# Kernel optimization log

Hardware: AMD Instinct MI355X
Metric: run time of the kernel (lower is better)

The kernel has to match this reference:

```python
import jax, jax.numpy as jnp
import numpy as np

DIM = 1024
N_SRC = 4096
N_TGT = 4096


def setup_inputs() -> dict:
    key = jax.random.key(0)
    ks = jax.random.split(key, 7)
    scale = 1.0 / np.sqrt(DIM)
    return {
        "source": jax.random.normal(ks[0], (N_SRC, DIM), dtype=jnp.float32),
        "target": jax.random.normal(ks[1], (N_TGT, DIM), dtype=jnp.float32),
        "W_src": jax.random.uniform(ks[2], (DIM, DIM), minval=-scale, maxval=scale, dtype=jnp.float32),
        "b_src": jax.random.uniform(ks[3], (DIM,), minval=-scale, maxval=scale, dtype=jnp.float32),
        "W_tgt": jax.random.uniform(ks[4], (DIM, DIM), minval=-scale, maxval=scale, dtype=jnp.float32),
        "b_tgt": jax.random.uniform(ks[5], (DIM,), minval=-scale, maxval=scale, dtype=jnp.float32),
        "temperature": jnp.array(1.0, dtype=jnp.float32),
    }


def reference(source, target, W_src, b_src, W_tgt, b_tgt, temperature):
    # Linear projections (torch Linear: x @ W.T + b)
    sp = source @ W_src.T + b_src            # [N, d]
    tp = target @ W_tgt.T + b_tgt            # [M, d]
    sq_s = jnp.sum(sp * sp, axis=-1, keepdims=True)   # [N, 1]
    sq_t = jnp.sum(tp * tp, axis=-1)                  # [M]
    d2 = sq_s + sq_t[None, :] - 2.0 * (sp @ tp.T)     # [N, M]
    cost = jnp.sqrt(jnp.maximum(d2, 0.0))
    # Softmin-style kernel, row-normalized over target entries
    K = jnp.exp(-cost / temperature)
    K = K / jnp.sum(K, axis=1, keepdims=True)
    aligned_source = K @ target                       # [N, d]
    return aligned_source, K
```

## Files before the change

### kernel.cpp

```cpp
#include <hip/hip_runtime.h>
#include <stdint.h>

#define DIM  1024
#define NSRC 4096
#define NTGT 4096

typedef __bf16 bf16_t;
typedef bf16_t bf16x8 __attribute__((ext_vector_type(8)));
typedef float  fx4    __attribute__((ext_vector_type(4)));

static __device__ __forceinline__ unsigned short f2bf(float f) {
  union { float f; uint32_t u; } v; v.f = f;
  return (unsigned short)((v.u + 0x7FFFu + ((v.u >> 16) & 1u)) >> 16);
}
static __device__ __forceinline__ float bf2f(unsigned short h) {
  union { uint32_t u; float f; } v; v.u = ((uint32_t)h) << 16;
  return v.f;
}

static __device__ __forceinline__ void gl_lds16(const unsigned short* g, unsigned short* l) {
  __builtin_amdgcn_global_load_lds(
      (__attribute__((address_space(1))) const void*)g,
      (__attribute__((address_space(3))) void*)l, 16, 0, 0);
}

typedef const __attribute__((address_space(3))) unsigned short* lds3p;

template <int IMM>
static __device__ __forceinline__ bf16x8 dsr128(lds3p p) {
  bf16x8 r;
  asm volatile("ds_read_b128 %0, %1 offset:%2" : "=v"(r) : "v"(p), "n"(IMM));
  return r;
}


__global__ void k_convert_all(const float* __restrict__ s, const float* __restrict__ t,
                              const float* __restrict__ w0, const float* __restrict__ w1,
                              unsigned short* __restrict__ sb, unsigned short* __restrict__ tb,
                              unsigned short* __restrict__ wb0, unsigned short* __restrict__ wb1) {
  int b = blockIdx.x;
  const float* in; unsigned short* out; int idx;
  if (b < 4096)      { in = s;  out = sb;  idx = b * 256 + threadIdx.x; }
  else if (b < 8192) { in = t;  out = tb;  idx = (b - 4096) * 256 + threadIdx.x; }
  else if (b < 9216) { in = w0; out = wb0; idx = (b - 8192) * 256 + threadIdx.x; }
  else               { in = w1; out = wb1; idx = (b - 9216) * 256 + threadIdx.x; }
  float4 v = ((const float4*)in)[idx];
  ushort4 o;
  o.x = f2bf(v.x); o.y = f2bf(v.y); o.z = f2bf(v.z); o.w = f2bf(v.w);
  ((ushort4*)out)[idx] = o;
}

__global__ void k_transpose_bf16(const float* __restrict__ in, unsigned short* __restrict__ out,
                                 int R, int C) {
  __shared__ unsigned short tile[32][33];
  int c0 = blockIdx.x * 32, r0 = blockIdx.y * 32;
  int tx = threadIdx.x, ty = threadIdx.y;
  for (int i = ty; i < 32; i += 8) {
    int row = r0 + i;
    int p = row & 63;
    int tr = (row & ~63) | ((p >> 2) | ((p & 3) << 4));
    tile[i][tx] = f2bf(in[(size_t)tr * C + c0 + tx]);
  }
  __syncthreads();
  for (int i = ty; i < 32; i += 8)
    out[(size_t)(c0 + i) * R + r0 + tx] = tile[tx][i];
}

__global__ void k_finalize_aligned(const float* __restrict__ P, float* __restrict__ aligned,
                                   const float* __restrict__ rs) {
  const int b = blockIdx.x;
  const int lane = threadIdx.x & 63, w = threadIdx.x >> 6;
  const int src = ((lane & 15) << 2) | (lane >> 4);
  const size_t stride = (size_t)NSRC * DIM;
#pragma unroll
  for (int it = 0; it < 4; ++it) {
    int idx = b * 16 + w * 4 + it;
    size_t base = (size_t)idx * 64;
    float r = 1.0f / rs[idx >> 4];
    float v = (P[base + lane] + P[base + stride + lane] +
               P[base + 2 * stride + lane] + P[base + 3 * stride + lane]) * r;
    aligned[base + lane] = __shfl(v, src, 64);
  }
}

__global__ void k_finalize_K(const unsigned short* __restrict__ Eb, float* __restrict__ Kf,
                             const float* __restrict__ rs) {
  const int b = blockIdx.x;
  const int lane = threadIdx.x & 63, w = threadIdx.x >> 6;
  const int src = ((lane & 15) << 2) | (lane >> 4);
#pragma unroll
  for (int it = 0; it < 8; ++it) {
    int idx = b * 32 + w * 8 + it;
    size_t base = (size_t)idx * 64;
    float r = 1.0f / rs[idx >> 6];
    float v = bf2f(Eb[base + lane]) * r;
    Kf[base + lane] = __shfl(v, src, 64);
  }
}

template <int EPI, int LDK>
__global__ void __launch_bounds__(512, 2)
k_tile256(const unsigned short* __restrict__ A0, const unsigned short* __restrict__ B0,
          const unsigned short* __restrict__ A1, const unsigned short* __restrict__ B1,
          const float* __restrict__ bias0, const float* __restrict__ bias1,
          unsigned short* __restrict__ Cb0, unsigned short* __restrict__ Cb1,
          unsigned short* __restrict__ Eb, float* __restrict__ Cf,
          const float* __restrict__ sqs, const float* __restrict__ sqt,
          const float* __restrict__ tempPtr,
          float* __restrict__ red0, float* __restrict__ red1) {
  __shared__ unsigned short ldsA[32768];
  __shared__ unsigned short ldsB[32768];

  const unsigned short* A = A0;
  const unsigned short* B = B0;
  const float* bias = bias0;
  unsigned short* Cb = Cb0;
  float* red = red0;
  if constexpr (EPI == 0) {
    if (blockIdx.z) { A = A1; B = B1; bias = bias1; Cb = Cb1; red = red1; }
  }
  if constexpr (EPI == 3) { A += blockIdx.z * 1024; B += blockIdx.z * 1024; }

  const int tid = threadIdx.x;
  const int lane = tid & 63, w = tid >> 6;
  const int wm = w >> 2, wn = w & 3;
  const int fr = lane & 15, kq = lane >> 4;
  const int m0 = blockIdx.y * 256, n0 = blockIdx.x * 256;

  const int rin = lane >> 2;
  const int cs  = ((lane & 3) * 8) ^ ((lane >> 5) ? 16 : 0);
  const size_t aoff0 = (size_t)(m0 + w * 16 + rin) * LDK + cs;
  const size_t aoff1 = (size_t)(m0 + (8 + w) * 16 + rin) * LDK + cs;
  const size_t boff0 = (size_t)(n0 + w * 16 + rin) * LDK + cs;
  const size_t boff1 = (size_t)(n0 + (8 + w) * 16 + rin) * LDK + cs;

  const int roA = fr * 32 + ((kq * 8) ^ ((fr & 8) ? 16 : 0));
  const lds3p baseA = (lds3p)ldsA + wm * 4096 + roA;
  const lds3p baseB = (lds3p)ldsB + wn * 2048 + roA;

#define STAGE_A(buf, ksb, kk) do { \
    gl_lds16(A + aoff0 + (kk) + (ksb) * 32, ldsA + (buf) * 16384 + (ksb) * 8192 + w * 512); \
    gl_lds16(A + aoff1 + (kk) + (ksb) * 32, ldsA + (buf) * 16384 + (ksb) * 8192 + (8 + w) * 512); \
  } while (0)
#define STAGE_B(buf, ksb, kk) do { \
    gl_lds16(B + boff0 + (kk) + (ksb) * 32, ldsB + (buf) * 16384 + (ksb) * 8192 + w * 512); \
    gl_lds16(B + boff1 + (kk) + (ksb) * 32, ldsB + (buf) * 16384 + (ksb) * 8192 + (8 + w) * 512); \
  } while (0)

  const fx4 fz = {0.f, 0.f, 0.f, 0.f};
  fx4 acc[8][4];
#pragma unroll
  for (int i = 0; i < 8; ++i)
#pragma unroll
    for (int j = 0; j < 4; ++j) acc[i][j] = fz;

  bf16x8 a[8], b0v, b1v;

#define LDA1(buf, ks, i) a[i] = dsr128<(buf) * 32768 + (ks) * 16384 + (i) * 1024>(baseA)
#define LDA8(buf, ks) do { \
    LDA1(buf, ks, 0); LDA1(buf, ks, 1); LDA1(buf, ks, 2); LDA1(buf, ks, 3); \
    LDA1(buf, ks, 4); LDA1(buf, ks, 5); LDA1(buf, ks, 6); LDA1(buf, ks, 7); \
  } while (0)
#define LDB2(buf, ks, jh) do { \
    b0v = dsr128<(buf) * 32768 + (ks) * 16384 + (jh) * 2048>(baseB); \
    b1v = dsr128<(buf) * 32768 + (ks) * 16384 + (jh) * 2048 + 1024>(baseB); \
  } while (0)
#define MFMA16(jh) do { _Pragma("unroll") \
    for (int i = 0; i < 8; ++i) { \
      acc[i][(jh) * 2]     = __builtin_amdgcn_mfma_f32_16x16x32_bf16(a[i], b0v, acc[i][(jh) * 2], 0, 0, 0); \
      acc[i][(jh) * 2 + 1] = __builtin_amdgcn_mfma_f32_16x16x32_bf16(a[i], b1v, acc[i][(jh) * 2 + 1], 0, 0, 0); \
    } } while (0)
#define SB0()   __builtin_amdgcn_sched_barrier(0)
#define BARS()  do { SB0(); __builtin_amdgcn_s_barrier(); SB0(); } while (0)
#define LGKM0() do { asm volatile("s_waitcnt lgkmcnt(0)" ::: "memory"); SB0(); } while (0)
#define VM6()   asm volatile("s_waitcnt vmcnt(6)" ::: "memory")

  STAGE_A(0, 0, 0);  STAGE_B(0, 0, 0);  STAGE_A(0, 1, 0);  STAGE_B(0, 1, 0);
  STAGE_A(1, 0, 64); STAGE_B(1, 0, 64); STAGE_A(1, 1, 64);
  VM6();
  BARS();

#pragma unroll 1
  for (int it = 0; it < 8; ++it) {
    const int kk1 = it * 128 + 64;
    const int kk2 = (it * 128 + 128) & 1023;
    const int kk3 = (it * 128 + 192) & 1023;
    LDA8(0, 0); LDB2(0, 0, 0); STAGE_B(1, 1, kk1);
    BARS(); LGKM0();
    __builtin_amdgcn_s_setprio(1); MFMA16(0); __builtin_amdgcn_s_setprio(0);
    BARS();
    LDB2(0, 0, 1); STAGE_A(0, 0, kk2);
    BARS(); LGKM0();
    __builtin_amdgcn_s_setprio(1); MFMA16(1); __builtin_amdgcn_s_setprio(0);
    BARS();
    LDA8(0, 1); LDB2(0, 1, 0); STAGE_B(0, 0, kk2);
    BARS(); LGKM0();
    __builtin_amdgcn_s_setprio(1); MFMA16(0); __builtin_amdgcn_s_setprio(0);
    BARS();
    LDB2(0, 1, 1); STAGE_A(0, 1, kk2);
    BARS(); LGKM0();
    __builtin_amdgcn_s_setprio(1); MFMA16(1); __builtin_amdgcn_s_setprio(0);
    VM6();
    BARS();
    LDA8(1, 0); LDB2(1, 0, 0); STAGE_B(0, 1, kk2);
    BARS(); LGKM0();
    __builtin_amdgcn_s_setprio(1); MFMA16(0); __builtin_amdgcn_s_setprio(0);
    BARS();
    LDB2(1, 0, 1); STAGE_A(1, 0, kk3);
    BARS(); LGKM0();
    __builtin_amdgcn_s_setprio(1); MFMA16(1); __builtin_amdgcn_s_setprio(0);
    BARS();
    LDA8(1, 1); LDB2(1, 1, 0); STAGE_B(1, 0, kk3);
    BARS(); LGKM0();
    __builtin_amdgcn_s_setprio(1); MFMA16(0); __builtin_amdgcn_s_setprio(0);
    BARS();
    LDB2(1, 1, 1); STAGE_A(1, 1, kk3);
    BARS(); LGKM0();
    __builtin_amdgcn_s_setprio(1); MFMA16(1); __builtin_amdgcn_s_setprio(0);
    VM6();
    BARS();
  }
  asm volatile("s_waitcnt vmcnt(0)" ::: "memory");
  __syncthreads();

  const int gcol0 = n0 + wn * 64 + fr;
  const int scol  = n0 + wn * 64 + fr * 4;

  if constexpr (EPI == 0) {
#pragma unroll
    for (int i = 0; i < 8; ++i)
#pragma unroll
      for (int r = 0; r < 4; ++r) {
        const int gm = m0 + wm * 128 + i * 16 + kq * 4 + r;
        float racc = 0.f;
        ushort4 o; unsigned short* op = (unsigned short*)&o;
#pragma unroll
        for (int j = 0; j < 4; ++j) {
          float e = acc[i][j][r] + bias[gcol0 + j * 16];
          unsigned short eb = f2bf(e);
          op[j] = eb;
          float ev = bf2f(eb);
          racc += ev * ev;
        }
        *(ushort4*)(Cb + (size_t)gm * DIM + scol) = o;
        racc += __shfl_xor(racc, 1, 64);
        racc += __shfl_xor(racc, 2, 64);
        racc += __shfl_xor(racc, 4, 64);
        racc += __shfl_xor(racc, 8, 64);
        if (fr == 0) atomicAdd(&red[gm], racc);
      }
  } else if constexpr (EPI == 1) {
    const float invT = 1.0f / tempPtr[0];
#pragma unroll
    for (int i = 0; i < 8; ++i)
#pragma unroll
      for (int r = 0; r < 4; ++r) {
        const int gm = m0 + wm * 128 + i * 16 + kq * 4 + r;
        const float si = sqs[gm];
        float racc = 0.f;
        ushort4 o; unsigned short* op = (unsigned short*)&o;
#pragma unroll
        for (int j = 0; j < 4; ++j) {
          float d2 = si + sqt[gcol0 + j * 16] - 2.0f * acc[i][j][r];
          float c = sqrtf(fmaxf(d2, 0.0f));
          unsigned short eb = f2bf(__expf(-c * invT));
          op[j] = eb;
          racc += bf2f(eb);
        }
        *(ushort4*)(Eb + (size_t)gm * NTGT + scol) = o;
        racc += __shfl_xor(racc, 1, 64);
        racc += __shfl_xor(racc, 2, 64);
        racc += __shfl_xor(racc, 4, 64);
        racc += __shfl_xor(racc, 8, 64);
        if (fr == 0) atomicAdd(&red[gm], racc);
      }
  } else {
    float* Pz = Cf + (size_t)blockIdx.z * NSRC * DIM;
#pragma unroll
    for (int i = 0; i < 8; ++i)
#pragma unroll
      for (int r = 0; r < 4; ++r) {
        const int gm = m0 + wm * 128 + i * 16 + kq * 4 + r;
        float4 v = make_float4(acc[i][0][r], acc[i][1][r], acc[i][2][r], acc[i][3][r]);
        *(float4*)(Pz + (size_t)gm * DIM + scol) = v;
      }
  }
#undef STAGE_A
#undef STAGE_B
#undef LDA1
#undef LDA8
#undef LDB2
#undef MFMA16
#undef SB0
#undef BARS
#undef LGKM0
#undef VM6
}

extern "C" void kernel_launch(void* const* d_in, const int* in_sizes, int n_in,
                              void* d_out, int out_size, void* d_ws, size_t ws_size,
                              hipStream_t stream) {
  const float* source = (const float*)d_in[0];
  const float* target = (const float*)d_in[1];
  const float* W_src  = (const float*)d_in[2];
  const float* b_src  = (const float*)d_in[3];
  const float* W_tgt  = (const float*)d_in[4];
  const float* b_tgt  = (const float*)d_in[5];
  const float* temp   = (const float*)d_in[6];

  float* out     = (float*)d_out;
  float* aligned = out;
  float* Kout    = out + (size_t)NSRC * DIM;
  float* parts   = Kout;

  char* ws = (char*)d_ws;
  unsigned short* src_b  = (unsigned short*)(ws + 0);
  unsigned short* tgt_b  = (unsigned short*)(ws + 8388608);
  unsigned short* Wsrc_b = (unsigned short*)(ws + 16777216);
  unsigned short* Wtgt_b = (unsigned short*)(ws + 18874368);
  unsigned short* sp_b   = (unsigned short*)(ws + 20971520);
  unsigned short* tp_b   = (unsigned short*)(ws + 29360128);
  unsigned short* tgtT_b = (unsigned short*)(ws + 37748736);
  unsigned short* E_b    = (unsigned short*)(ws + 46137344);
  float* sq_s  = (float*)(ws + 79691776);
  float* sq_t  = (float*)(ws + 79708160);
  float* rsums = (float*)(ws + 79724544);

  hipMemsetAsync(sq_s, 0, 3 * NSRC * sizeof(float), stream);

  k_convert_all<<<10240, 256, 0, stream>>>(source, target, W_src, W_tgt,
                                           src_b, tgt_b, Wsrc_b, Wtgt_b);
  k_transpose_bf16<<<dim3(DIM / 32, NTGT / 32), dim3(32, 8), 0, stream>>>(target, tgtT_b, NTGT, DIM);

  k_tile256<0, DIM><<<dim3(DIM / 256, NSRC / 256, 2), 512, 0, stream>>>(
      src_b, Wsrc_b, tgt_b, Wtgt_b, b_src, b_tgt, sp_b, tp_b,
      nullptr, nullptr, nullptr, nullptr, nullptr, sq_s, sq_t);

  k_tile256<1, DIM><<<dim3(NTGT / 256, NSRC / 256, 1), 512, 0, stream>>>(
      sp_b, tp_b, nullptr, nullptr, nullptr, nullptr, nullptr, nullptr,
      E_b, nullptr, sq_s, sq_t, temp, rsums, nullptr);

  k_tile256<3, NTGT><<<dim3(DIM / 256, NSRC / 256, 4), 512, 0, stream>>>(
      E_b, tgtT_b, nullptr, nullptr, nullptr, nullptr, nullptr, nullptr,
      nullptr, parts, nullptr, nullptr, nullptr, nullptr, nullptr);

  k_finalize_aligned<<<4096, 256, 0, stream>>>(parts, aligned, rsums);
  k_finalize_K<<<8192, 256, 0, stream>>>(E_b, Kout, rsums);
}
```

Before: 276.7 us.

## Restructure GEMM main loop into four phases and remap blocks for XCD locality

The main k-loop goes from eight half-phases, each bracketed by barriers, to four phases. Each phase loads all four B fragments plus eight A fragments, issues both A and B stage copies, waits on lgkmcnt(2) to start the first MFMA half early, then finishes with lgkmcnt(0). This halves the barrier count and overlaps the second B read with compute, at the cost of two extra B registers and a changed vmcnt depth. Block IDs are also permuted so that consecutive tiles spread across the eight XCDs in a chunked order, aiming for better L2 reuse.

```diff
diff --git a/kernel.cpp b/kernel.cpp
--- a/kernel.cpp
+++ b/kernel.cpp
@@ -121,11 +121,20 @@
   }
   if constexpr (EPI == 3) { A += blockIdx.z * 1024; B += blockIdx.z * 1024; }
 
+  int nbx = blockIdx.x, nby = blockIdx.y;
+  {
+    const int nx = gridDim.x, n = gridDim.x * gridDim.y;
+    const int id = nby * nx + nbx;
+    const int q = n >> 3;
+    const int s = (id & 7) * q + (id >> 3);
+    nbx = s % nx; nby = s / nx;
+  }
+
   const int tid = threadIdx.x;
   const int lane = tid & 63, w = tid >> 6;
   const int wm = w >> 2, wn = w & 3;
   const int fr = lane & 15, kq = lane >> 4;
-  const int m0 = blockIdx.y * 256, n0 = blockIdx.x * 256;
+  const int m0 = nby * 256, n0 = nbx * 256;
 
   const int rin = lane >> 2;
   const int cs  = ((lane & 3) * 8) ^ ((lane >> 5) ? 16 : 0);
@@ -154,30 +163,42 @@
 #pragma unroll
     for (int j = 0; j < 4; ++j) acc[i][j] = fz;
 
-  bf16x8 a[8], b0v, b1v;
+  bf16x8 a[8], b0v, b1v, b2v, b3v;
 
 #define LDA1(buf, ks, i) a[i] = dsr128<(buf) * 32768 + (ks) * 16384 + (i) * 1024>(baseA)
 #define LDA8(buf, ks) do { \
     LDA1(buf, ks, 0); LDA1(buf, ks, 1); LDA1(buf, ks, 2); LDA1(buf, ks, 3); \
     LDA1(buf, ks, 4); LDA1(buf, ks, 5); LDA1(buf, ks, 6); LDA1(buf, ks, 7); \
   } while (0)
-#define LDB2(buf, ks, jh) do { \
-    b0v = dsr128<(buf) * 32768 + (ks) * 16384 + (jh) * 2048>(baseB); \
-    b1v = dsr128<(buf) * 32768 + (ks) * 16384 + (jh) * 2048 + 1024>(baseB); \
-  } while (0)
-#define MFMA16(jh) do { _Pragma("unroll") \
+#define LDB2(buf, ks, jh, r0, r1) do { \
+    r0 = dsr128<(buf) * 32768 + (ks) * 16384 + (jh) * 2048>(baseB); \
+    r1 = dsr128<(buf) * 32768 + (ks) * 16384 + (jh) * 2048 + 1024>(baseB); \
+  } while (0)
+#define MFMA16(jh, r0, r1) do { _Pragma("unroll") \
     for (int i = 0; i < 8; ++i) { \
-      acc[i][(jh) * 2]     = __builtin_amdgcn_mfma_f32_16x16x32_bf16(a[i], b0v, acc[i][(jh) * 2], 0, 0, 0); \
-      acc[i][(jh) * 2 + 1] = __builtin_amdgcn_mfma_f32_16x16x32_bf16(a[i], b1v, acc[i][(jh) * 2 + 1], 0, 0, 0); \
+      acc[i][(jh) * 2]     = __builtin_amdgcn_mfma_f32_16x16x32_bf16(a[i], r0, acc[i][(jh) * 2], 0, 0, 0); \
+      acc[i][(jh) * 2 + 1] = __builtin_amdgcn_mfma_f32_16x16x32_bf16(a[i], r1, acc[i][(jh) * 2 + 1], 0, 0, 0); \
     } } while (0)
 #define SB0()   __builtin_amdgcn_sched_barrier(0)
 #define BARS()  do { SB0(); __builtin_amdgcn_s_barrier(); SB0(); } while (0)
+#define LGKM2() do { asm volatile("s_waitcnt lgkmcnt(2)" ::: "memory"); SB0(); } while (0)
 #define LGKM0() do { asm volatile("s_waitcnt lgkmcnt(0)" ::: "memory"); SB0(); } while (0)
-#define VM6()   asm volatile("s_waitcnt vmcnt(6)" ::: "memory")
+#define VM4()   asm volatile("s_waitcnt vmcnt(4)" ::: "memory")
+
+#define PHASE(buf, ks, sb, sk, kk) do { \
+    LDB2(buf, ks, 0, b0v, b1v); LDA8(buf, ks); LDB2(buf, ks, 1, b2v, b3v); \
+    STAGE_A(sb, sk, kk); STAGE_B(sb, sk, kk); \
+    BARS(); LGKM2(); \
+    __builtin_amdgcn_s_setprio(1); \
+    MFMA16(0, b0v, b1v); \
+    LGKM0(); \
+    MFMA16(1, b2v, b3v); \
+    __builtin_amdgcn_s_setprio(0); \
+  } while (0)
 
   STAGE_A(0, 0, 0);  STAGE_B(0, 0, 0);  STAGE_A(0, 1, 0);  STAGE_B(0, 1, 0);
-  STAGE_A(1, 0, 64); STAGE_B(1, 0, 64); STAGE_A(1, 1, 64);
-  VM6();
+  STAGE_A(1, 0, 64); STAGE_B(1, 0, 64);
+  VM4();
   BARS();
 
 #pragma unroll 1
@@ -185,39 +206,15 @@
     const int kk1 = it * 128 + 64;
     const int kk2 = (it * 128 + 128) & 1023;
     const int kk3 = (it * 128 + 192) & 1023;
-    LDA8(0, 0); LDB2(0, 0, 0); STAGE_B(1, 1, kk1);
-    BARS(); LGKM0();
-    __builtin_amdgcn_s_setprio(1); MFMA16(0); __builtin_amdgcn_s_setprio(0);
+    PHASE(0, 0, 1, 1, kk1);
     BARS();
-    LDB2(0, 0, 1); STAGE_A(0, 0, kk2);
-    BARS(); LGKM0();
-    __builtin_amdgcn_s_setprio(1); MFMA16(1); __builtin_amdgcn_s_setprio(0);
+    PHASE(0, 1, 0, 0, kk2);
+    VM4();
     BARS();
-    LDA8(0, 1); LDB2(0, 1, 0); STAGE_B(0, 0, kk2);
-    BARS(); LGKM0();
-    __builtin_amdgcn_s_setprio(1); MFMA16(0); __builtin_amdgcn_s_setprio(0);
+    PHASE(1, 0, 0, 1, kk2);
     BARS();
-    LDB2(0, 1, 1); STAGE_A(0, 1, kk2);
-    BARS(); LGKM0();
-    __builtin_amdgcn_s_setprio(1); MFMA16(1); __builtin_amdgcn_s_setprio(0);
-    VM6();
-    BARS();
-    LDA8(1, 0); LDB2(1, 0, 0); STAGE_B(0, 1, kk2);
-    BARS(); LGKM0();
-    __builtin_amdgcn_s_setprio(1); MFMA16(0); __builtin_amdgcn_s_setprio(0);
-    BARS();
-    LDB2(1, 0, 1); STAGE_A(1, 0, kk3);
-    BARS(); LGKM0();
-    __builtin_amdgcn_s_setprio(1); MFMA16(1); __builtin_amdgcn_s_setprio(0);
-    BARS();
-    LDA8(1, 1); LDB2(1, 1, 0); STAGE_B(1, 0, kk3);
-    BARS(); LGKM0();
-    __builtin_amdgcn_s_setprio(1); MFMA16(0); __builtin_amdgcn_s_setprio(0);
-    BARS();
-    LDB2(1, 1, 1); STAGE_A(1, 1, kk3);
-    BARS(); LGKM0();
-    __builtin_amdgcn_s_setprio(1); MFMA16(1); __builtin_amdgcn_s_setprio(0);
-    VM6();
+    PHASE(1, 1, 1, 0, kk3);
+    VM4();
     BARS();
   }
   asm volatile("s_waitcnt vmcnt(0)" ::: "memory");
@@ -291,10 +288,12 @@
 #undef LDA8
 #undef LDB2
 #undef MFMA16
+#undef PHASE
 #undef SB0
 #undef BARS
+#undef LGKM2
 #undef LGKM0
-#undef VM6
+#undef VM4
 }
 
 extern "C" void kernel_launch(void* const* d_in, const int* in_sizes, int n_in,
```

New measurement: 276.7 us. Within noise of the previous version (-0.0%).
